# Optimization experiments

Hardware: AMD Instinct MI355X
Metric: run time of the kernel (lower is better)

## Reference

```python
import jax, jax.numpy as jnp
import numpy as np

N_ITER = 4  # n_iter
NEG = -1e9  # masked-score fill (softmax-safe stand-in for -inf)


def _mfvi(x, mask, ternary, global_):
    """MFVI message passing between head (H) and node (Z) variables with global nodes.

    x:       [B, L, D] unary scores for Z nodes
    mask:    [B, L]    padding mask (nonzero = valid token)
    ternary: [D, D, H] ternary factor scores f(Z_i=a, Z_j=b, H-channel c)
    global_: [G, D, H] global-node factor scores
    Defaults: norm=softmax, regularize=1, stepsize=1, damping=0, async_update,
    no tensor decomposition, mode='all-attn', block_msg=False, output_prob=False.
    """
    B, L, D = x.shape
    m1 = (mask != 0)                                             # [B, L]
    pair_valid = m1[:, None, :, None] & m1[:, None, None, :]     # [B, 1, L, L]
    unary = x                                                    # pos_embed='none'
    Qz = jax.nn.softmax(unary, axis=-1)                          # [B, L, D]
    F_Z = unary
    neg = jnp.asarray(NEG, x.dtype)
    for _ in range(N_ITER):
        # --- H update: scores for head variable H_{i,c} over candidate heads j ---
        # F_Hs[n,h,i,j] = sum_{a,b} Qz[n,i,a] * ternary[a,b,h] * Qz[n,j,b]
        F_Hs = jnp.einsum('nia,abh,njb->nhij', Qz, ternary, Qz)  # [B, H, L, L]
        F_Hs = jnp.where(pair_valid, F_Hs, neg)
        # global-node columns: F_Hg[n,h,i,g] = sum_a Qz[n,i,a] * global_[g,a,h]
        F_Hg = jnp.einsum('nia,gah->nhig', Qz, global_)          # [B, H, L, G]
        F_H = jnp.concatenate([F_Hs, F_Hg], axis=-1)             # [B, H, L, L+G]
        Q_H = jax.nn.softmax(F_H, axis=-1)                       # regularize_H = 1
        Qhs, Qhg = Q_H[..., :L], Q_H[..., L:]
        # --- Z update (async: uses fresh Q_H) ---
        # message to Z_i from its chosen head j
        msg_i = jnp.einsum('nhij,njb,abh->nia', Qhs, Qz, ternary)
        # message to Z_j from dependents i (block_msg=False keeps it)
        msg_j = jnp.einsum('nhij,nia,abh->njb', Qhs, Qz, ternary)
        # message to Z_i from global nodes
        msg_g = jnp.einsum('nhig,gah->nia', Qhg, global_)
        F_Z = unary + msg_i + msg_j + msg_g                      # [B, L, D]
        Qz = jax.nn.softmax(F_Z, axis=-1)                        # regularize_Z = 1
    # output_prob=False -> unnormalized scores, zeroed at padding
    return jnp.where(m1[..., None], F_Z, jnp.zeros_like(F_Z))


def setup_inputs() -> dict:
    key = jax.random.key(0)
    k1, k2, k3 = jax.random.split(key, 3)
    B, L, D, H, G = 4, 1024, 128, 8, 64
    x = jax.random.normal(k1, (B, L, D), dtype=jnp.float32)
    mask = jnp.ones((B, L), dtype=jnp.int32)
    ternary = jax.random.normal(k2, (D, D, H), dtype=jnp.float32)          # init std=1
    global_ = jax.random.normal(k3, (G, D, H), dtype=jnp.float32) / np.sqrt(D)
    return {"x": x, "mask": mask, "ternary": ternary, "global_": global_}


def reference(x, mask, ternary, global_):
    return _mfvi(x, mask, ternary, global_)
```

## Files before the change

kernel.cpp:

```cpp
#include <hip/hip_runtime.h>
#include <math.h>

#define Bn 4
#define Ln 1024
#define Dn 128
#define Hn 8
#define Gn 64
#define NITERS 4

typedef _Float16 f16;
typedef _Float16 half8 __attribute__((ext_vector_type(8)));
typedef _Float16 half4v __attribute__((ext_vector_type(4)));
typedef float floatx4 __attribute__((ext_vector_type(4)));

#define WPAD 136

#define MFMA(a, b, c) __builtin_amdgcn_mfma_f32_16x16x32_f16((a), (b), (c), 0, 0, 0)

union h8u { half8 h; half4v v[2]; };

__device__ __forceinline__ void gl_lds16(const f16* g, f16* l) {
    __builtin_amdgcn_global_load_lds(
        (const __attribute__((address_space(1))) void*)(g),
        (__attribute__((address_space(3))) void*)(l),
        16, 0, 0);
}

__device__ __forceinline__ void issue_tiles8(const f16* us, const f16* ub, int sb,
                                             f16* UsB, f16* UbB, int w, int l) {
    #pragma unroll
    for (int k = 0; k < 2; k++) {
        int c = w * 2 + k;
        {
            int r = c * 4 + (l >> 4); int g = (l & 15) ^ (r & 7);
            gl_lds16(us + (size_t)r * Dn + g * 8, UsB + c * 512);
        }
        {
            int r = c * 8 + (l >> 3); int g = (l & 7) ^ (r & 7);
            gl_lds16(ub + (size_t)r * sb + g * 8, UbB + c * 512);
        }
    }
}

__device__ __forceinline__ void bar_vm4() {
    asm volatile("s_waitcnt vmcnt(4)" ::: "memory");
    __builtin_amdgcn_s_barrier();
    __builtin_amdgcn_sched_barrier(0);
}
__device__ __forceinline__ void bar_vm0() {
    asm volatile("s_waitcnt vmcnt(0)" ::: "memory");
    __builtin_amdgcn_s_barrier();
    __builtin_amdgcn_sched_barrier(0);
}

__global__ void repack_kernel(const float* __restrict__ ter, const float* __restrict__ glb,
                              f16* __restrict__ TpA, f16* __restrict__ TpB,
                              f16* __restrict__ GpA, f16* __restrict__ Gpt) {
    int idx = blockIdx.x * 256 + threadIdx.x;
    if (idx < Dn * Dn * Hn) {
        int h = idx % Hn; int b = (idx / Hn) % Dn; int a = idx / (Hn * Dn);
        f16 v = (f16)ter[idx];
        TpA[((size_t)h * Dn + a) * Dn + b] = v;
        TpB[((size_t)h * Dn + b) * Dn + a] = v;
    }
    if (idx < Gn * Dn * Hn) {
        int h = idx % Hn; int a = (idx / Hn) % Dn; int g = idx / (Hn * Dn);
        f16 v = (f16)glb[idx];
        GpA[((size_t)h * Gn + g) * Dn + a] = v;
        int pos = ((g >> 5) << 5) | (((g >> 2) & 3) << 3) | (((g >> 4) & 1) << 2) | (g & 3);
        Gpt[((size_t)h * Dn + a) * Gn + pos] = v;
    }
}

__global__ void softmax_rows_kernel(const float* __restrict__ in, f16* __restrict__ out) {
    int row = blockIdx.x;
    int t = threadIdx.x;
    __shared__ float red[2];
    float v = in[(size_t)row * Dn + t];
    float m = v;
    #pragma unroll
    for (int off = 1; off < 64; off <<= 1) m = fmaxf(m, __shfl_xor(m, off, 64));
    if ((t & 63) == 0) red[t >> 6] = m;
    __syncthreads();
    m = fmaxf(red[0], red[1]);
    float e = __expf(v - m);
    float s = e;
    #pragma unroll
    for (int off = 1; off < 64; off <<= 1) s += __shfl_xor(s, off, 64);
    __syncthreads();
    if ((t & 63) == 0) red[t >> 6] = s;
    __syncthreads();
    s = red[0] + red[1];
    out[(size_t)row * Dn + t] = (f16)(e / s);
}

__launch_bounds__(256, 4)
__global__ void uv_kernel(const f16* __restrict__ Qz, const f16* __restrict__ TpA,
                          const f16* __restrict__ TpB, const int* __restrict__ mask,
                          f16* __restrict__ U, f16* __restrict__ Ut, f16* __restrict__ Vt) {
    int bx = blockIdx.x;
    int h  = blockIdx.y;
    int n  = blockIdx.z;
    int t  = threadIdx.x;
    int w = t >> 6, l = t & 63, m = l & 15, q = l >> 4;

    __shared__ __align__(16) f16 Ts[128 * WPAD];

    int jrow = bx * 64 + w * 16 + m;
    const f16* qbase = Qz + ((size_t)n * Ln + jrow) * Dn;
    half8 aq[4];
    #pragma unroll
    for (int ks = 0; ks < 4; ks++)
        aq[ks] = *(const half8*)(qbase + ks * 32 + q * 8);

    size_t hoff = (size_t)(n * Hn + h);
    int jr0 = bx * 64 + w * 16 + 4 * q;
    int jrp = bx * 64 + (w >> 1) * 32 + q * 8 + (w & 1) * 4;

    float bias[4];
    #pragma unroll
    for (int reg = 0; reg < 4; reg++)
        bias[reg] = mask[n * Ln + jr0 + reg] ? 0.f : -64.f;

    {
        const f16* src = TpA + (size_t)h * Dn * Dn;
        for (int ii = 0; ii < 8; ii++) {
            int idx = t + 256 * ii; int r = idx >> 4, c = idx & 15;
            *(float4*)&Ts[r * WPAD + c * 8] = *(const float4*)(src + (size_t)r * Dn + c * 8);
        }
        __syncthreads();
        #pragma unroll
        for (int ct = 0; ct < 8; ct++) {
            floatx4 acc = {0.f, 0.f, 0.f, 0.f};
            #pragma unroll
            for (int ks = 0; ks < 4; ks++) {
                half8 b = *(const half8*)&Ts[(ct * 16 + m) * WPAD + ks * 32 + q * 8];
                acc = MFMA(aq[ks], b, acc);
            }
            f16* ub = U + (hoff * Ln + jr0) * Dn + ct * 16 + m;
            half4v pk;
            #pragma unroll
            for (int reg = 0; reg < 4; reg++) {
                f16 v = (f16)(acc[reg] + bias[reg]);
                ub[(size_t)reg * Dn] = v;
                pk[reg] = v;
            }
            *(half4v*)(Ut + (hoff * Dn + ct * 16 + m) * Ln + jrp) = pk;
        }
        __syncthreads();
    }
    {
        const f16* src = TpB + (size_t)h * Dn * Dn;
        for (int ii = 0; ii < 8; ii++) {
            int idx = t + 256 * ii; int r = idx >> 4, c = idx & 15;
            *(float4*)&Ts[r * WPAD + c * 8] = *(const float4*)(src + (size_t)r * Dn + c * 8);
        }
        __syncthreads();
        #pragma unroll
        for (int ct = 0; ct < 8; ct++) {
            floatx4 acc = {0.f, 0.f, 0.f, 0.f};
            #pragma unroll
            for (int ks = 0; ks < 4; ks++) {
                half8 b = *(const half8*)&Ts[(ct * 16 + m) * WPAD + ks * 32 + q * 8];
                acc = MFMA(aq[ks], b, acc);
            }
            half4v pk = { (f16)acc[0], (f16)acc[1], (f16)acc[2], (f16)acc[3] };
            *(half4v*)(Vt + (hoff * Dn + ct * 16 + m) * Ln + jrp) = pk;
        }
    }
}

__launch_bounds__(512, 1)
__global__ void msgi_kernel(const f16* __restrict__ Qz, const f16* __restrict__ U,
                            const f16* __restrict__ Ut, const f16* __restrict__ GpA,
                            const f16* __restrict__ Gpt, const int* __restrict__ mask,
                            f16* __restrict__ Macc, float* __restrict__ rowLinv) {
    int p = blockIdx.x;
    int h  = p & 7;
    int it = (p >> 3) & 7;
    int n  = p >> 6;
    int t = threadIdx.x;
    int w = t >> 6, l = t & 63, m = l & 15, q = l >> 4;
    int ih = w >> 1;
    int kw = w & 1;

    __shared__ __align__(16) f16 Us[3][64 * 128];
    __shared__ __align__(16) f16 Ub[3][128 * 64];
    __shared__ float lredS[2][128];
    __shared__ float linvS[128];

    half8 bq[2][4];
    #pragma unroll
    for (int ib = 0; ib < 2; ib++) {
        const f16* qr = Qz + ((size_t)n * Ln + it * 128 + ih * 32 + ib * 16 + m) * Dn;
        #pragma unroll
        for (int ks = 0; ks < 4; ks++)
            bq[ib][ks] = *(const half8*)(qr + ks * 32 + q * 8);
    }

    float lacc[2] = {0.f, 0.f};
    floatx4 Oacc[2][8];
    #pragma unroll
    for (int ib = 0; ib < 2; ib++)
        #pragma unroll
        for (int at = 0; at < 8; at++) Oacc[ib][at] = (floatx4){0.f, 0.f, 0.f, 0.f};

    size_t hoff = (size_t)(n * Hn + h);

    issue_tiles8(U + hoff * Ln * Dn, Ut + hoff * Dn * Ln, Ln, Us[0], Ub[0], w, l);
    issue_tiles8(U + (hoff * Ln + 64) * Dn, Ut + hoff * Dn * Ln + 64, Ln, Us[1], Ub[1], w, l);
    bar_vm4();

    for (int jt = 0; jt < 17; jt++) {
        int cur = jt % 3;
        if (jt + 2 <= 16) {
            int nb = (jt + 2) % 3;
            const f16 *us, *ub; int sb;
            if (jt + 2 < 16) {
                us = U + (hoff * Ln + (size_t)(jt + 2) * 64) * Dn;
                ub = Ut + hoff * Dn * Ln + (jt + 2) * 64;
                sb = Ln;
            } else {
                us = GpA + (size_t)h * Gn * Dn;
                ub = Gpt + (size_t)h * Dn * Gn;
                sb = Gn;
            }
            issue_tiles8(us, ub, sb, Us[nb], Ub[nb], w, l);
        }
        half4v hv[2][2];
        #pragma unroll
        for (int jb2 = 0; jb2 < 2; jb2++) {
            int jb = kw * 2 + jb2;
            int r0 = jb * 16 + m;
            half8 au[4];
            #pragma unroll
            for (int ks = 0; ks < 4; ks++)
                au[ks] = *(const half8*)&Us[cur][((size_t)r0 << 7) + ((((ks << 2) + q)) ^ (r0 & 7)) * 8];
            #pragma unroll
            for (int ib = 0; ib < 2; ib++) {
                floatx4 s = {0.f, 0.f, 0.f, 0.f};
                #pragma unroll
                for (int ks = 0; ks < 4; ks++) s = MFMA(au[ks], bq[ib][ks], s);
                half4v pk;
                #pragma unroll
                for (int reg = 0; reg < 4; reg++) {
                    float p2 = __expf(fminf(s[reg], 11.f));
                    lacc[ib] += p2;
                    pk[reg] = (f16)p2;
                }
                hv[jb2][ib] = pk;
            }
        }
        half8 aP[2];
        #pragma unroll
        for (int ib = 0; ib < 2; ib++) {
            h8u u; u.v[0] = hv[0][ib]; u.v[1] = hv[1][ib];
            aP[ib] = u.h;
        }
        #pragma unroll
        for (int at = 0; at < 8; at++) {
            int r0 = at * 16 + m;
            half8 bU = *(const half8*)&Ub[cur][((size_t)r0 << 6) + ((((kw << 2) + q)) ^ (r0 & 7)) * 8];
            #pragma unroll
            for (int ib = 0; ib < 2; ib++)
                Oacc[ib][at] = MFMA(aP[ib], bU, Oacc[ib][at]);
        }
        if (jt < 15) bar_vm4(); else bar_vm0();
    }

    #pragma unroll
    for (int ib = 0; ib < 2; ib++) {
        float v = lacc[ib];
        v += __shfl_xor(v, 16, 64);
        v += __shfl_xor(v, 32, 64);
        lacc[ib] = v;
    }
    if (q == 0) {
        lredS[kw][ih * 32 + m]      = lacc[0];
        lredS[kw][ih * 32 + 16 + m] = lacc[1];
    }
    __syncthreads();
    size_t rbase = hoff * Ln + (size_t)it * 128;
    if (t < 128) {
        float inv = 1.0f / (lredS[0][t] + lredS[1][t]);
        linvS[t] = inv;
        rowLinv[rbase + t] = mask[n * Ln + it * 128 + t] ? inv : 0.f;
    }
    {
        float* od = (ih < 3) ? ((float*)Us + (size_t)ih * 4096) : (float*)Ub;
        od += (size_t)l * 64;
        if (kw == 1) {
            #pragma unroll
            for (int c = 0; c < 16; c++)
                *(floatx4*)(od + c * 4) = Oacc[c >> 3][c & 7];
        }
        __syncthreads();
        if (kw == 0) {
            f16* Mo = Macc + rbase * Dn;
            #pragma unroll
            for (int ib = 0; ib < 2; ib++)
                #pragma unroll
                for (int reg = 0; reg < 4; reg++) {
                    int row = ih * 32 + ib * 16 + 4 * q + reg;
                    float inv = linvS[row];
                    #pragma unroll
                    for (int at = 0; at < 8; at++) {
                        float v = Oacc[ib][at][reg] + od[(ib * 8 + at) * 4 + reg];
                        Mo[(size_t)row * Dn + at * 16 + m] = (f16)(v * inv);
                    }
                }
        }
    }
}

__launch_bounds__(512, 1)
__global__ void msgj_kernel(const f16* __restrict__ Qz, const f16* __restrict__ U,
                            const f16* __restrict__ Vt, const int* __restrict__ mask,
                            const float* __restrict__ rowLinv, f16* __restrict__ Macc) {
    int p = blockIdx.x;
    int h  = p & 7;
    int jt = (p >> 3) & 7;
    int n  = p >> 6;
    int t = threadIdx.x;
    int w = t >> 6, l = t & 63, m = l & 15, q = l >> 4;
    int jh = w >> 1;
    int kw = w & 1;

    __shared__ __align__(16) f16 Qs[3][64 * 128];
    __shared__ __align__(16) f16 Vb[3][128 * 64];
    __shared__ __align__(16) float lvAll[Ln];

    size_t hoff = (size_t)(n * Hn + h);

    half8 bu[2][4];
    #pragma unroll
    for (int jb = 0; jb < 2; jb++) {
        const f16* ur = U + (hoff * Ln + (size_t)jt * 128 + jh * 32 + jb * 16 + m) * Dn;
        #pragma unroll
        for (int ks = 0; ks < 4; ks++)
            bu[jb][ks] = *(const half8*)(ur + ks * 32 + q * 8);
    }

    floatx4 Oacc[2][8];
    #pragma unroll
    for (int jb = 0; jb < 2; jb++)
        #pragma unroll
        for (int bt = 0; bt < 8; bt++) Oacc[jb][bt] = (floatx4){0.f, 0.f, 0.f, 0.f};

    lvAll[t]       = rowLinv[hoff * Ln + t];
    lvAll[t + 512] = rowLinv[hoff * Ln + t + 512];

    issue_tiles8(Qz + (size_t)n * Ln * Dn, Vt + hoff * Dn * Ln, Ln, Qs[0], Vb[0], w, l);
    issue_tiles8(Qz + ((size_t)n * Ln + 64) * Dn, Vt + hoff * Dn * Ln + 64, Ln, Qs[1], Vb[1], w, l);
    asm volatile("s_waitcnt vmcnt(4) lgkmcnt(0)" ::: "memory");
    __builtin_amdgcn_s_barrier();
    __builtin_amdgcn_sched_barrier(0);

    for (int it2 = 0; it2 < 16; it2++) {
        int cur = it2 % 3;
        if (it2 + 2 < 16) {
            int nb = (it2 + 2) % 3;
            issue_tiles8(Qz + ((size_t)n * Ln + (size_t)(it2 + 2) * 64) * Dn,
                         Vt + hoff * Dn * Ln + (it2 + 2) * 64, Ln, Qs[nb], Vb[nb], w, l);
        }
        half4v hv[2][2];
        #pragma unroll
        for (int ib2 = 0; ib2 < 2; ib2++) {
            int ibt = kw * 2 + ib2;
            int r0 = ibt * 16 + m;
            half8 aq2[4];
            #pragma unroll
            for (int ks = 0; ks < 4; ks++)
                aq2[ks] = *(const half8*)&Qs[cur][((size_t)r0 << 7) + ((((ks << 2) + q)) ^ (r0 & 7)) * 8];
            float4 lv = *(const float4*)&lvAll[it2 * 64 + ibt * 16 + 4 * q];
            float lv4[4] = { lv.x, lv.y, lv.z, lv.w };
            #pragma unroll
            for (int jb = 0; jb < 2; jb++) {
                floatx4 s = {0.f, 0.f, 0.f, 0.f};
                #pragma unroll
                for (int ks = 0; ks < 4; ks++) s = MFMA(aq2[ks], bu[jb][ks], s);
                half4v pk;
                #pragma unroll
                for (int reg = 0; reg < 4; reg++)
                    pk[reg] = (f16)(__expf(fminf(s[reg], 11.f)) * lv4[reg]);
                hv[ib2][jb] = pk;
            }
        }
        half8 aP[2];
        #pragma unroll
        for (int jb = 0; jb < 2; jb++) {
            h8u u; u.v[0] = hv[0][jb]; u.v[1] = hv[1][jb];
            aP[jb] = u.h;
        }
        #pragma unroll
        for (int bt = 0; bt < 8; bt++) {
            int r0 = bt * 16 + m;
            half8 bV = *(const half8*)&Vb[cur][((size_t)r0 << 6) + ((((kw << 2) + q)) ^ (r0 & 7)) * 8];
            #pragma unroll
            for (int jb = 0; jb < 2; jb++)
                Oacc[jb][bt] = MFMA(aP[jb], bV, Oacc[jb][bt]);
        }
        if (it2 < 14) bar_vm4(); else bar_vm0();
    }

    {
        float* od = (jh < 3) ? ((float*)Qs + (size_t)jh * 4096) : (float*)Vb;
        od += (size_t)l * 64;
        if (kw == 1) {
            #pragma unroll
            for (int c = 0; c < 16; c++)
                *(floatx4*)(od + c * 4) = Oacc[c >> 3][c & 7];
        }
        __syncthreads();
        if (kw == 0) {
            f16* Mo = Macc + (hoff * Ln + (size_t)jt * 128) * Dn;
            #pragma unroll
            for (int jb = 0; jb < 2; jb++)
                #pragma unroll
                for (int reg = 0; reg < 4; reg++) {
                    int row = jh * 32 + jb * 16 + 4 * q + reg;
                    #pragma unroll
                    for (int bt = 0; bt < 8; bt++) {
                        f16* p2 = &Mo[(size_t)row * Dn + bt * 16 + m];
                        float v = Oacc[jb][bt][reg] + od[(jb * 8 + bt) * 4 + reg];
                        *p2 = (f16)((float)*p2 + v);
                    }
                }
        }
    }
}

__global__ void combine_kernel(const float* __restrict__ x, const f16* __restrict__ Macc,
                               const int* __restrict__ mask, float* __restrict__ out,
                               f16* __restrict__ Qzh, int do_softmax, int do_mask) {
    int row = blockIdx.x;
    int t = threadIdx.x;
    __shared__ float red[2];
    int n = row >> 10;
    float acc = x[(size_t)row * Dn + t];
    const f16* mp = Macc + (size_t)n * Hn * Ln * Dn + (size_t)(row & 1023) * Dn + t;
    #pragma unroll
    for (int h = 0; h < Hn; h++) acc += (float)mp[(size_t)h * Ln * Dn];
    float o = acc;
    if (do_mask && mask[row] == 0) o = 0.f;
    out[(size_t)row * Dn + t] = o;
    if (do_softmax) {
        float m = acc;
        #pragma unroll
        for (int off = 1; off < 64; off <<= 1) m = fmaxf(m, __shfl_xor(m, off, 64));
        if ((t & 63) == 0) red[t >> 6] = m;
        __syncthreads();
        m = fmaxf(red[0], red[1]);
        float e = __expf(acc - m);
        float s = e;
        #pragma unroll
        for (int off = 1; off < 64; off <<= 1) s += __shfl_xor(s, off, 64);
        __syncthreads();
        if ((t & 63) == 0) red[t >> 6] = s;
        __syncthreads();
        s = red[0] + red[1];
        Qzh[(size_t)row * Dn + t] = (f16)(e / s);
    }
}

extern "C" void kernel_launch(void* const* d_in, const int* in_sizes, int n_in,
                              void* d_out, int out_size, void* d_ws, size_t ws_size,
                              hipStream_t stream) {
    const float* x       = (const float*)d_in[0];
    const int*   mask    = (const int*)d_in[1];
    const float* ternary = (const float*)d_in[2];
    const float* global_ = (const float*)d_in[3];
    float* out = (float*)d_out;
    (void)ws_size; (void)n_in; (void)in_sizes; (void)out_size;

    char* ws = (char*)d_ws;
    size_t o = 0;
    f16* Qzh = (f16*)(ws + o); o += (size_t)Bn * Ln * Dn * 2;
    f16* U   = (f16*)(ws + o); o += (size_t)Bn * Hn * Ln * Dn * 2;
    f16* Ut  = (f16*)(ws + o); o += (size_t)Bn * Hn * Ln * Dn * 2;
    f16* Vt  = (f16*)(ws + o); o += (size_t)Bn * Hn * Ln * Dn * 2;
    f16* TpA = (f16*)(ws + o); o += (size_t)Hn * Dn * Dn * 2;
    f16* TpB = (f16*)(ws + o); o += (size_t)Hn * Dn * Dn * 2;
    f16* GpA = (f16*)(ws + o); o += (size_t)Hn * Gn * Dn * 2;
    f16* Gpt = (f16*)(ws + o); o += (size_t)Hn * Dn * Gn * 2;
    float* rowLinv = (float*)(ws + o); o += (size_t)Bn * Hn * Ln * 4;
    f16* Macc = (f16*)(ws + o); o += (size_t)Bn * Hn * Ln * Dn * 2;

    repack_kernel<<<(Dn * Dn * Hn + 255) / 256, 256, 0, stream>>>(ternary, global_, TpA, TpB, GpA, Gpt);
    softmax_rows_kernel<<<Bn * Ln, 128, 0, stream>>>(x, Qzh);

    for (int it = 0; it < NITERS; it++) {
        uv_kernel<<<dim3(Ln / 64, Hn, Bn), 256, 0, stream>>>(Qzh, TpA, TpB, mask, U, Ut, Vt);
        msgi_kernel<<<dim3(Ln / 128 * Hn * Bn), 512, 0, stream>>>(Qzh, U, Ut, GpA, Gpt, mask, Macc, rowLinv);
        msgj_kernel<<<dim3(Ln / 128 * Hn * Bn), 512, 0, stream>>>(Qzh, U, Vt, mask, rowLinv, Macc);
        combine_kernel<<<Bn * Ln, 128, 0, stream>>>(x, Macc, mask, out, Qzh,
                                                    (it < NITERS - 1) ? 1 : 0,
                                                    (it == NITERS - 1) ? 1 : 0);
    }
}
```

Baseline: 389.0 us.

## Split msgi/msgj reductions into two halves with partial sums combined later

Both message kernels now split their reduction dimension into two halves, doubling the grid from 256 to 512 blocks. msgi writes unnormalized partial outputs and partial row sums, and msgj computes the inverse normalizer from both partials. The combine kernel sums the partial Mi/Mj buffers and applies the normalization. Pipelining drops from triple to double buffering with plain __syncthreads, which shrinks LDS so two blocks fit per CU (launch_bounds 512,2). This removes msgj's read-modify-write of Macc, but adds more workspace traffic in combine and a less aggressive prefetch.

```diff
diff --git a/kernel.cpp b/kernel.cpp
--- a/kernel.cpp
+++ b/kernel.cpp
@@ -40,17 +40,6 @@
             gl_lds16(ub + (size_t)r * sb + g * 8, UbB + c * 512);
         }
     }
-}
-
-__device__ __forceinline__ void bar_vm4() {
-    asm volatile("s_waitcnt vmcnt(4)" ::: "memory");
-    __builtin_amdgcn_s_barrier();
-    __builtin_amdgcn_sched_barrier(0);
-}
-__device__ __forceinline__ void bar_vm0() {
-    asm volatile("s_waitcnt vmcnt(0)" ::: "memory");
-    __builtin_amdgcn_s_barrier();
-    __builtin_amdgcn_sched_barrier(0);
 }
 
 __global__ void repack_kernel(const float* __restrict__ ter, const float* __restrict__ glb,
@@ -170,24 +159,26 @@
     }
 }
 
-__launch_bounds__(512, 1)
+__launch_bounds__(512, 2)
 __global__ void msgi_kernel(const f16* __restrict__ Qz, const f16* __restrict__ U,
                             const f16* __restrict__ Ut, const f16* __restrict__ GpA,
-                            const f16* __restrict__ Gpt, const int* __restrict__ mask,
-                            f16* __restrict__ Macc, float* __restrict__ rowLinv) {
+                            const f16* __restrict__ Gpt,
+                            f16* __restrict__ Mi, float* __restrict__ rowLp) {
     int p = blockIdx.x;
-    int h  = p & 7;
-    int it = (p >> 3) & 7;
-    int n  = p >> 6;
+    int h     = p & 7;
+    int jhalf = (p >> 3) & 1;
+    int it    = (p >> 4) & 7;
+    int n     = p >> 7;
     int t = threadIdx.x;
     int w = t >> 6, l = t & 63, m = l & 15, q = l >> 4;
     int ih = w >> 1;
     int kw = w & 1;
 
-    __shared__ __align__(16) f16 Us[3][64 * 128];
-    __shared__ __align__(16) f16 Ub[3][128 * 64];
-    __shared__ float lredS[2][128];
-    __shared__ float linvS[128];
+    __shared__ __align__(16) f16 Us[2][64 * 128];
+    __shared__ __align__(16) f16 Ub[2][128 * 64];
+    __shared__ float lred[2][128];
+
+    size_t hoff = (size_t)(n * Hn + h);
 
     half8 bq[2][4];
     #pragma unroll
@@ -205,27 +196,28 @@
         #pragma unroll
         for (int at = 0; at < 8; at++) Oacc[ib][at] = (floatx4){0.f, 0.f, 0.f, 0.f};
 
-    size_t hoff = (size_t)(n * Hn + h);
-
-    issue_tiles8(U + hoff * Ln * Dn, Ut + hoff * Dn * Ln, Ln, Us[0], Ub[0], w, l);
-    issue_tiles8(U + (hoff * Ln + 64) * Dn, Ut + hoff * Dn * Ln + 64, Ln, Us[1], Ub[1], w, l);
-    bar_vm4();
-
-    for (int jt = 0; jt < 17; jt++) {
-        int cur = jt % 3;
-        if (jt + 2 <= 16) {
-            int nb = (jt + 2) % 3;
+    int NS = 8 + jhalf;
+    int jt0 = jhalf * 8;
+
+    issue_tiles8(U + (hoff * Ln + (size_t)jt0 * 64) * Dn,
+                 Ut + hoff * Dn * Ln + jt0 * 64, Ln, Us[0], Ub[0], w, l);
+    __syncthreads();
+
+    for (int s = 0; s < NS; s++) {
+        int cur = s & 1, nxt = cur ^ 1;
+        if (s + 1 < NS) {
+            int jt1 = jt0 + s + 1;
             const f16 *us, *ub; int sb;
-            if (jt + 2 < 16) {
-                us = U + (hoff * Ln + (size_t)(jt + 2) * 64) * Dn;
-                ub = Ut + hoff * Dn * Ln + (jt + 2) * 64;
+            if (jt1 < 16) {
+                us = U + (hoff * Ln + (size_t)jt1 * 64) * Dn;
+                ub = Ut + hoff * Dn * Ln + jt1 * 64;
                 sb = Ln;
             } else {
                 us = GpA + (size_t)h * Gn * Dn;
                 ub = Gpt + (size_t)h * Dn * Gn;
                 sb = Gn;
             }
-            issue_tiles8(us, ub, sb, Us[nb], Ub[nb], w, l);
+            issue_tiles8(us, ub, sb, Us[nxt], Ub[nxt], w, l);
         }
         half4v hv[2][2];
         #pragma unroll
@@ -238,13 +230,13 @@
                 au[ks] = *(const half8*)&Us[cur][((size_t)r0 << 7) + ((((ks << 2) + q)) ^ (r0 & 7)) * 8];
             #pragma unroll
             for (int ib = 0; ib < 2; ib++) {
-                floatx4 s = {0.f, 0.f, 0.f, 0.f};
+                floatx4 s2 = {0.f, 0.f, 0.f, 0.f};
                 #pragma unroll
-                for (int ks = 0; ks < 4; ks++) s = MFMA(au[ks], bq[ib][ks], s);
+                for (int ks = 0; ks < 4; ks++) s2 = MFMA(au[ks], bq[ib][ks], s2);
                 half4v pk;
                 #pragma unroll
                 for (int reg = 0; reg < 4; reg++) {
-                    float p2 = __expf(fminf(s[reg], 11.f));
+                    float p2 = __expf(fminf(s2[reg], 11.f));
                     lacc[ib] += p2;
                     pk[reg] = (f16)p2;
                 }
@@ -265,7 +257,7 @@
             for (int ib = 0; ib < 2; ib++)
                 Oacc[ib][at] = MFMA(aP[ib], bU, Oacc[ib][at]);
         }
-        if (jt < 15) bar_vm4(); else bar_vm0();
+        __syncthreads();
     }
 
     #pragma unroll
@@ -276,59 +268,54 @@
         lacc[ib] = v;
     }
     if (q == 0) {
-        lredS[kw][ih * 32 + m]      = lacc[0];
-        lredS[kw][ih * 32 + 16 + m] = lacc[1];
-    }
-    __syncthreads();
-    size_t rbase = hoff * Ln + (size_t)it * 128;
-    if (t < 128) {
-        float inv = 1.0f / (lredS[0][t] + lredS[1][t]);
-        linvS[t] = inv;
-        rowLinv[rbase + t] = mask[n * Ln + it * 128 + t] ? inv : 0.f;
-    }
-    {
-        float* od = (ih < 3) ? ((float*)Us + (size_t)ih * 4096) : (float*)Ub;
-        od += (size_t)l * 64;
-        if (kw == 1) {
-            #pragma unroll
-            for (int c = 0; c < 16; c++)
-                *(floatx4*)(od + c * 4) = Oacc[c >> 3][c & 7];
-        }
-        __syncthreads();
-        if (kw == 0) {
-            f16* Mo = Macc + rbase * Dn;
-            #pragma unroll
-            for (int ib = 0; ib < 2; ib++)
+        lred[kw][ih * 32 + m]      = lacc[0];
+        lred[kw][ih * 32 + 16 + m] = lacc[1];
+    }
+    __syncthreads();
+    if (t < 128)
+        rowLp[((size_t)jhalf * Bn * Hn + hoff) * Ln + it * 128 + t] = lred[0][t] + lred[1][t];
+    float* od = (ih < 2) ? ((float*)Us + (size_t)ih * 4096)
+                         : ((float*)Ub + (size_t)(ih - 2) * 4096);
+    od += (size_t)l * 64;
+    if (kw == 1) {
+        #pragma unroll
+        for (int c = 0; c < 16; c++)
+            *(floatx4*)(od + c * 4) = Oacc[c >> 3][c & 7];
+    }
+    __syncthreads();
+    if (kw == 0) {
+        f16* Mo = Mi + (((size_t)jhalf * Bn * Hn + hoff) * Ln + (size_t)it * 128) * Dn;
+        #pragma unroll
+        for (int ib = 0; ib < 2; ib++)
+            #pragma unroll
+            for (int reg = 0; reg < 4; reg++) {
+                int row = ih * 32 + ib * 16 + 4 * q + reg;
                 #pragma unroll
-                for (int reg = 0; reg < 4; reg++) {
-                    int row = ih * 32 + ib * 16 + 4 * q + reg;
-                    float inv = linvS[row];
-                    #pragma unroll
-                    for (int at = 0; at < 8; at++) {
-                        float v = Oacc[ib][at][reg] + od[(ib * 8 + at) * 4 + reg];
-                        Mo[(size_t)row * Dn + at * 16 + m] = (f16)(v * inv);
-                    }
+                for (int at = 0; at < 8; at++) {
+                    float v = Oacc[ib][at][reg] + od[(ib * 8 + at) * 4 + reg];
+                    Mo[(size_t)row * Dn + at * 16 + m] = (f16)v;
                 }
-        }
-    }
-}
-
-__launch_bounds__(512, 1)
+            }
+    }
+}
+
+__launch_bounds__(512, 2)
 __global__ void msgj_kernel(const f16* __restrict__ Qz, const f16* __restrict__ U,
                             const f16* __restrict__ Vt, const int* __restrict__ mask,
-                            const float* __restrict__ rowLinv, f16* __restrict__ Macc) {
+                            const float* __restrict__ rowLp, f16* __restrict__ Mj) {
     int p = blockIdx.x;
-    int h  = p & 7;
-    int jt = (p >> 3) & 7;
-    int n  = p >> 6;
+    int h     = p & 7;
+    int ihalf = (p >> 3) & 1;
+    int jt    = (p >> 4) & 7;
+    int n     = p >> 7;
     int t = threadIdx.x;
     int w = t >> 6, l = t & 63, m = l & 15, q = l >> 4;
     int jh = w >> 1;
     int kw = w & 1;
 
-    __shared__ __align__(16) f16 Qs[3][64 * 128];
-    __shared__ __align__(16) f16 Vb[3][128 * 64];
-    __shared__ __align__(16) float lvAll[Ln];
+    __shared__ __align__(16) f16 Qs[2][64 * 128];
+    __shared__ __align__(16) f16 Vb[2][128 * 64];
+    __shared__ __align__(16) float lvAll[512];
 
     size_t hoff = (size_t)(n * Hn + h);
 
@@ -347,21 +334,24 @@
         #pragma unroll
         for (int bt = 0; bt < 8; bt++) Oacc[jb][bt] = (floatx4){0.f, 0.f, 0.f, 0.f};
 
-    lvAll[t]       = rowLinv[hoff * Ln + t];
-    lvAll[t + 512] = rowLinv[hoff * Ln + t + 512];
-
-    issue_tiles8(Qz + (size_t)n * Ln * Dn, Vt + hoff * Dn * Ln, Ln, Qs[0], Vb[0], w, l);
-    issue_tiles8(Qz + ((size_t)n * Ln + 64) * Dn, Vt + hoff * Dn * Ln + 64, Ln, Qs[1], Vb[1], w, l);
-    asm volatile("s_waitcnt vmcnt(4) lgkmcnt(0)" ::: "memory");
-    __builtin_amdgcn_s_barrier();
-    __builtin_amdgcn_sched_barrier(0);
-
-    for (int it2 = 0; it2 < 16; it2++) {
-        int cur = it2 % 3;
-        if (it2 + 2 < 16) {
-            int nb = (it2 + 2) % 3;
-            issue_tiles8(Qz + ((size_t)n * Ln + (size_t)(it2 + 2) * 64) * Dn,
-                         Vt + hoff * Dn * Ln + (it2 + 2) * 64, Ln, Qs[nb], Vb[nb], w, l);
+    {
+        int gi = ihalf * 512 + t;
+        float l0 = rowLp[hoff * Ln + gi];
+        float l1 = rowLp[((size_t)Bn * Hn + hoff) * Ln + gi];
+        lvAll[t] = mask[n * Ln + gi] ? 1.0f / (l0 + l1) : 0.f;
+    }
+
+    int gi0 = ihalf * 8;
+    issue_tiles8(Qz + ((size_t)n * Ln + (size_t)gi0 * 64) * Dn,
+                 Vt + hoff * Dn * Ln + gi0 * 64, Ln, Qs[0], Vb[0], w, l);
+    __syncthreads();
+
+    for (int s = 0; s < 8; s++) {
+        int cur = s & 1, nxt = cur ^ 1;
+        if (s + 1 < 8) {
+            int gi1 = gi0 + s + 1;
+            issue_tiles8(Qz + ((size_t)n * Ln + (size_t)gi1 * 64) * Dn,
+                         Vt + hoff * Dn * Ln + gi1 * 64, Ln, Qs[nxt], Vb[nxt], w, l);
         }
         half4v hv[2][2];
         #pragma unroll
@@ -372,17 +362,17 @@
             #pragma unroll
             for (int ks = 0; ks < 4; ks++)
                 aq2[ks] = *(const half8*)&Qs[cur][((size_t)r0 << 7) + ((((ks << 2) + q)) ^ (r0 & 7)) * 8];
-            float4 lv = *(const float4*)&lvAll[it2 * 64 + ibt * 16 + 4 * q];
+            float4 lv = *(const float4*)&lvAll[s * 64 + ibt * 16 + 4 * q];
             float lv4[4] = { lv.x, lv.y, lv.z, lv.w };
             #pragma unroll
             for (int jb = 0; jb < 2; jb++) {
-                floatx4 s = {0.f, 0.f, 0.f, 0.f};
+                floatx4 s2 = {0.f, 0.f, 0.f, 0.f};
                 #pragma unroll
-                for (int ks = 0; ks < 4; ks++) s = MFMA(aq2[ks], bu[jb][ks], s);
+                for (int ks = 0; ks < 4; ks++) s2 = MFMA(aq2[ks], bu[jb][ks], s2);
                 half4v pk;
                 #pragma unroll
                 for (int reg = 0; reg < 4; reg++)
-                    pk[reg] = (f16)(__expf(fminf(s[reg], 11.f)) * lv4[reg]);
+                    pk[reg] = (f16)(__expf(fminf(s2[reg], 11.f)) * lv4[reg]);
                 hv[ib2][jb] = pk;
             }
         }
@@ -400,47 +390,57 @@
             for (int jb = 0; jb < 2; jb++)
                 Oacc[jb][bt] = MFMA(aP[jb], bV, Oacc[jb][bt]);
         }
-        if (it2 < 14) bar_vm4(); else bar_vm0();
-    }
-
-    {
-        float* od = (jh < 3) ? ((float*)Qs + (size_t)jh * 4096) : (float*)Vb;
-        od += (size_t)l * 64;
-        if (kw == 1) {
-            #pragma unroll
-            for (int c = 0; c < 16; c++)
-                *(floatx4*)(od + c * 4) = Oacc[c >> 3][c & 7];
-        }
-        __syncthreads();
-        if (kw == 0) {
-            f16* Mo = Macc + (hoff * Ln + (size_t)jt * 128) * Dn;
-            #pragma unroll
-            for (int jb = 0; jb < 2; jb++)
+        __syncthreads();
+    }
+
+    float* od = (jh < 2) ? ((float*)Qs + (size_t)jh * 4096)
+                         : ((float*)Vb + (size_t)(jh - 2) * 4096);
+    od += (size_t)l * 64;
+    if (kw == 1) {
+        #pragma unroll
+        for (int c = 0; c < 16; c++)
+            *(floatx4*)(od + c * 4) = Oacc[c >> 3][c & 7];
+    }
+    __syncthreads();
+    if (kw == 0) {
+        f16* Mo = Mj + (((size_t)ihalf * Bn * Hn + hoff) * Ln + (size_t)jt * 128) * Dn;
+        #pragma unroll
+        for (int jb = 0; jb < 2; jb++)
+            #pragma unroll
+            for (int reg = 0; reg < 4; reg++) {
+                int row = jh * 32 + jb * 16 + 4 * q + reg;
                 #pragma unroll
-                for (int reg = 0; reg < 4; reg++) {
-                    int row = jh * 32 + jb * 16 + 4 * q + reg;
-                    #pragma unroll
-                    for (int bt = 0; bt < 8; bt++) {
-                        f16* p2 = &Mo[(size_t)row * Dn + bt * 16 + m];
-                        float v = Oacc[jb][bt][reg] + od[(jb * 8 + bt) * 4 + reg];
-                        *p2 = (f16)((float)*p2 + v);
-                    }
+                for (int bt = 0; bt < 8; bt++) {
+                    float v = Oacc[jb][bt][reg] + od[(jb * 8 + bt) * 4 + reg];
+                    Mo[(size_t)row * Dn + bt * 16 + m] = (f16)v;
                 }
-        }
-    }
-}
-
-__global__ void combine_kernel(const float* __restrict__ x, const f16* __restrict__ Macc,
+            }
+    }
+}
+
+__global__ void combine_kernel(const float* __restrict__ x, const f16* __restrict__ Mi,
+                               const f16* __restrict__ Mj, const float* __restrict__ rowLp,
                                const int* __restrict__ mask, float* __restrict__ out,
                                f16* __restrict__ Qzh, int do_softmax, int do_mask) {
     int row = blockIdx.x;
     int t = threadIdx.x;
     __shared__ float red[2];
     int n = row >> 10;
+    int r = row & 1023;
+    const size_t BH = (size_t)Bn * Hn;
     float acc = x[(size_t)row * Dn + t];
-    const f16* mp = Macc + (size_t)n * Hn * Ln * Dn + (size_t)(row & 1023) * Dn + t;
-    #pragma unroll
-    for (int h = 0; h < Hn; h++) acc += (float)mp[(size_t)h * Ln * Dn];
+    #pragma unroll
+    for (int h = 0; h < Hn; h++) {
+        size_t hoff = (size_t)n * Hn + h;
+        float l0 = rowLp[hoff * Ln + r];
+        float l1 = rowLp[(BH + hoff) * Ln + r];
+        float linv = 1.0f / (l0 + l1);
+        size_t o0 = (hoff * Ln + r) * Dn + t;
+        size_t o1 = ((BH + hoff) * Ln + r) * Dn + t;
+        float mi = (float)Mi[o0] + (float)Mi[o1];
+        float mj = (float)Mj[o0] + (float)Mj[o1];
+        acc += mi * linv + mj;
+    }
     float o = acc;
     if (do_mask && mask[row] == 0) o = 0.f;
     out[(size_t)row * Dn + t] = o;
@@ -483,17 +483,18 @@
     f16* TpB = (f16*)(ws + o); o += (size_t)Hn * Dn * Dn * 2;
     f16* GpA = (f16*)(ws + o); o += (size_t)Hn * Gn * Dn * 2;
     f16* Gpt = (f16*)(ws + o); o += (size_t)Hn * Dn * Gn * 2;
-    float* rowLinv = (float*)(ws + o); o += (size_t)Bn * Hn * Ln * 4;
-    f16* Macc = (f16*)(ws + o); o += (size_t)Bn * Hn * Ln * Dn * 2;
+    float* rowLp = (float*)(ws + o); o += (size_t)2 * Bn * Hn * Ln * 4;
+    f16* Mi  = (f16*)(ws + o); o += (size_t)2 * Bn * Hn * Ln * Dn * 2;
+    f16* Mj  = (f16*)(ws + o); o += (size_t)2 * Bn * Hn * Ln * Dn * 2;
 
     repack_kernel<<<(Dn * Dn * Hn + 255) / 256, 256, 0, stream>>>(ternary, global_, TpA, TpB, GpA, Gpt);
     softmax_rows_kernel<<<Bn * Ln, 128, 0, stream>>>(x, Qzh);
 
     for (int it = 0; it < NITERS; it++) {
         uv_kernel<<<dim3(Ln / 64, Hn, Bn), 256, 0, stream>>>(Qzh, TpA, TpB, mask, U, Ut, Vt);
-        msgi_kernel<<<dim3(Ln / 128 * Hn * Bn), 512, 0, stream>>>(Qzh, U, Ut, GpA, Gpt, mask, Macc, rowLinv);
-        msgj_kernel<<<dim3(Ln / 128 * Hn * Bn), 512, 0, stream>>>(Qzh, U, Vt, mask, rowLinv, Macc);
-        combine_kernel<<<Bn * Ln, 128, 0, stream>>>(x, Macc, mask, out, Qzh,
+        msgi_kernel<<<dim3(Ln / 128 * 2 * Hn * Bn), 512, 0, stream>>>(Qzh, U, Ut, GpA, Gpt, Mi, rowLp);
+        msgj_kernel<<<dim3(Ln / 128 * 2 * Hn * Bn), 512, 0, stream>>>(Qzh, U, Vt, mask, rowLp, Mj);
+        combine_kernel<<<Bn * Ln, 128, 0, stream>>>(x, Mi, Mj, rowLp, mask, out, Qzh,
                                                     (it < NITERS - 1) ? 1 : 0,
                                                     (it == NITERS - 1) ? 1 : 0);
     }
```

Measured after the change: 458.7 us. 1.18x slower.
